# Performance work log

Hardware: AMD Instinct MI355X
Metric: run time of the kernel (lower is better)

The kernel has to match this reference:

```python
import jax, jax.numpy as jnp
import numpy as np

EMBED_DIM = 768
NUM_HEADS = 12
HEAD_DIM = EMBED_DIM // NUM_HEADS
WINDOW = 64
B, S = 2, 2048


def setup_inputs() -> dict:
    key = jax.random.key(0)
    ks = jax.random.split(key, 8)
    xavier = 0.1 * np.sqrt(6.0 / (EMBED_DIM + EMBED_DIM))  # xavier_uniform with gain=0.1
    def lin_w(k):
        return jax.random.uniform(k, (EMBED_DIM, EMBED_DIM), jnp.float32, -xavier, xavier)
    return {
        "query": jax.random.normal(ks[0], (B, S, EMBED_DIM), jnp.float32),
        "key": jax.random.normal(ks[1], (B, S, EMBED_DIM), jnp.float32),
        "value": jax.random.normal(ks[2], (B, S, EMBED_DIM), jnp.float32),
        "key_padding_mask": jnp.zeros((B, S), dtype=bool),
        "Wq": lin_w(ks[3]), "bq": jnp.zeros((EMBED_DIM,), jnp.float32),
        "Wk": lin_w(ks[4]), "bk": jnp.zeros((EMBED_DIM,), jnp.float32),
        "Wv": lin_w(ks[5]), "bv": jnp.zeros((EMBED_DIM,), jnp.float32),
        "Wo": lin_w(ks[6]), "bo": jnp.zeros((EMBED_DIM,), jnp.float32),
    }


def reference(query, key, value, key_padding_mask, Wq, bq, Wk, bk, Wv, bv, Wo, bo):
    Bsz, Sl, E = query.shape
    H, D = NUM_HEADS, HEAD_DIM

    def proj(x, W, b):  # nn.Linear: x @ W.T + b, then split heads -> [B,H,S,D]
        return (x @ W.T + b).reshape(Bsz, Sl, H, D).transpose(0, 2, 1, 3)

    q = proj(query, Wq, bq)
    k = proj(key, Wk, bk)
    v = proj(value, Wv, bv)

    scale = float(D) ** -0.5
    scores = jnp.einsum("bhqd,bhkd->bhqk", q, k) * scale  # [B,H,S,S]

    idx = jnp.arange(Sl)
    win_mask = jnp.abs(idx[:, None] - idx[None, :]) > WINDOW  # True = masked out
    scores = jnp.where(win_mask[None, None], -10000.0, scores)
    scores = jnp.where(key_padding_mask[:, None, None, :], -10000.0, scores)
    scores = jnp.where(jnp.isnan(scores), -10000.0, scores)

    attn = jax.nn.softmax(scores, axis=-1) + 1e-6
    attn = jnp.where(jnp.isnan(attn), 1.0 / Sl, attn)

    ctx = jnp.einsum("bhqk,bhkd->bhqd", attn, v)
    ctx = ctx.transpose(0, 2, 1, 3).reshape(Bsz, Sl, E)
    out = ctx @ Wo.T + bo
    out = jnp.where(jnp.isnan(out), value, out)
    return out, attn
```

## Files before the change

kernel.cpp:

```cpp
#include <hip/hip_runtime.h>
#include <hip/hip_bf16.h>

#define EMBED 768
#define NHEADS 12
#define HDIM 64
#define WIN 64
#define BATCH 2
#define SEQ 2048
#define MROWS (BATCH*SEQ)
#define NBH (BATCH*NHEADS)
#define QT 32
#define KP 160
#define KPAD 168
#define SPAD 164

typedef __attribute__((ext_vector_type(8))) short short8;
typedef __attribute__((ext_vector_type(4))) float f32x4;

__device__ __forceinline__ float bf2f(unsigned short u) {
    union { unsigned int i; float f; } z;
    z.i = ((unsigned int)u) << 16;
    return z.f;
}
__device__ __forceinline__ unsigned short f2bf(float f) {
    __hip_bfloat16 h = __float2bfloat16(f);
    return *reinterpret_cast<unsigned short*>(&h);
}

__device__ __forceinline__ void gload16(const void* g, void* l) {
    __builtin_amdgcn_global_load_lds(
        (const __attribute__((address_space(1))) unsigned int*)g,
        (__attribute__((address_space(3))) unsigned int*)l,
        16, 0, 0);
}

struct CvtArgs {
    const float* src[4];
    unsigned short* dst[4];
};

__global__ __launch_bounds__(256) void cvt_w(CvtArgs ca) {
    const int n4 = EMBED * EMBED / 4;
    const int bper = (n4 + 255) / 256;
    int seg = blockIdx.x / bper;
    int i = (blockIdx.x - seg * bper) * 256 + threadIdx.x;
    if (i < n4) {
        float4 v = reinterpret_cast<const float4*>(ca.src[seg])[i];
        ushort4 o;
        o.x = f2bf(v.x); o.y = f2bf(v.y); o.z = f2bf(v.z); o.w = f2bf(v.w);
        reinterpret_cast<ushort4*>(ca.dst[seg])[i] = o;
    }
}

struct GArgs {
    const void* A[3];
    const unsigned short* Bm[3];
    const float* bias[3];
    void* C[3];
};

template<int F32OUT, int F32A>
__global__ __launch_bounds__(256) void gemm_nt(GArgs ga, int M, int N, int K) {
    const int NPANEL = gridDim.y * gridDim.z;
    const int flat = (blockIdx.z * gridDim.y + blockIdx.y) * gridDim.x + blockIdx.x;
    const int xcd = flat & 7;
    const int j = flat >> 3;
    const int panel = xcd * (NPANEL >> 3) + j / gridDim.x;
    const int z = panel / gridDim.y;
    const int bm = (panel % gridDim.y) * 128;
    const int bn = (j % gridDim.x) * 128;

    const unsigned short* __restrict__ Bm = ga.Bm[z];
    const float* __restrict__ bias = ga.bias[z];

    __shared__ alignas(16) unsigned char AsRaw[F32A ? 128 * 32 * 4 : 128 * 32 * 2];
    __shared__ unsigned short Bs[128 * 32];

    const int tid = threadIdx.x;
    const int lane = tid & 63;
    const int wid = tid >> 6;
    const int wm = wid >> 1, wn = wid & 1;

    f32x4 acc[4][4] = {};

    const int fr = lane & 15;
    const int krow = (lane >> 4) * 8;

    for (int k0 = 0; k0 < K; k0 += 32) {
        if (F32A) {
            const float* Af = (const float*)ga.A[z];
            float* AsF = (float*)AsRaw;
#pragma unroll
            for (int it = 0; it < 4; ++it) {
                int idx = it * 256 + tid;
                int r = idx >> 3;
                int cc = idx & 7;
                int gcc = cc ^ (r & 7);
                gload16(Af + (size_t)(bm + r) * K + k0 + gcc * 4, &AsF[idx * 4]);
            }
        } else {
            const unsigned short* Ab = (const unsigned short*)ga.A[z];
#pragma unroll
            for (int it = 0; it < 2; ++it) {
                int idx = it * 256 + tid;
                int r = idx >> 2;
                int c = (idx & 3) * 8;
                gload16(Ab + (size_t)(bm + r) * K + k0 + c,
                        (unsigned short*)AsRaw + idx * 8);
            }
        }
#pragma unroll
        for (int it = 0; it < 2; ++it) {
            int idx = it * 256 + tid;
            int r = idx >> 2;
            int c = (idx & 3) * 8;
            gload16(Bm + (size_t)(bn + r) * K + k0 + c, &Bs[idx * 8]);
        }
        __syncthreads();

        short8 af[4], bfv[4];
#pragma unroll
        for (int mf = 0; mf < 4; ++mf) {
            int r = wm * 64 + mf * 16 + fr;
            if (F32A) {
                const float* AsF = (const float*)AsRaw;
                int kc0 = (lane >> 4) * 2;
                int s0 = kc0 ^ (r & 7);
                f32x4 v0 = *reinterpret_cast<const f32x4*>(&AsF[(r * 8 + s0) * 4]);
                f32x4 v1 = *reinterpret_cast<const f32x4*>(&AsF[(r * 8 + (s0 ^ 1)) * 4]);
                unsigned short* ou = reinterpret_cast<unsigned short*>(&af[mf]);
                ou[0] = f2bf(v0[0]); ou[1] = f2bf(v0[1]);
                ou[2] = f2bf(v0[2]); ou[3] = f2bf(v0[3]);
                ou[4] = f2bf(v1[0]); ou[5] = f2bf(v1[1]);
                ou[6] = f2bf(v1[2]); ou[7] = f2bf(v1[3]);
            } else {
                af[mf] = *reinterpret_cast<const short8*>(
                    (const unsigned short*)AsRaw + r * 32 + krow);
            }
        }
#pragma unroll
        for (int nf = 0; nf < 4; ++nf)
            bfv[nf] = *reinterpret_cast<const short8*>(&Bs[(wn * 64 + nf * 16 + fr) * 32 + krow]);
#pragma unroll
        for (int mf = 0; mf < 4; ++mf)
#pragma unroll
            for (int nf = 0; nf < 4; ++nf)
                acc[mf][nf] = __builtin_amdgcn_mfma_f32_16x16x32_bf16(
                    af[mf], bfv[nf], acc[mf][nf], 0, 0, 0);
        __syncthreads();
    }

    const int fq = lane >> 4;
#pragma unroll
    for (int mf = 0; mf < 4; ++mf)
#pragma unroll
        for (int nf = 0; nf < 4; ++nf) {
            int col = bn + wn * 64 + nf * 16 + fr;
            float bv = bias[col];
#pragma unroll
            for (int r = 0; r < 4; ++r) {
                int row = bm + wm * 64 + mf * 16 + fq * 4 + r;
                float v = acc[mf][nf][r] + bv;
                if (F32OUT)
                    reinterpret_cast<float*>(ga.C[z])[(size_t)row * N + col] = v;
                else
                    reinterpret_cast<unsigned short*>(ga.C[z])[(size_t)row * N + col] = f2bf(v);
            }
        }
}

__global__ __launch_bounds__(256) void sumv_kernel(const unsigned short* __restrict__ Vb,
                                                   float* __restrict__ sumV) {
    __shared__ float r[32][HDIM];
    const int bh = blockIdx.x;
    const int b = bh / NHEADS, h = bh % NHEADS;
    const int dg = (threadIdx.x & 7) * 8;
    const int r0 = threadIdx.x >> 3;
    float acc[8] = {};
    const unsigned short* vp = Vb + (size_t)(b * SEQ) * EMBED + h * HDIM + dg;
    for (int j = r0; j < SEQ; j += 32) {
        short8 v = *reinterpret_cast<const short8*>(vp + (size_t)j * EMBED);
#pragma unroll
        for (int e = 0; e < 8; ++e)
            acc[e] += bf2f(((const unsigned short*)&v)[e]);
    }
#pragma unroll
    for (int e = 0; e < 8; ++e) r[r0][dg + e] = acc[e];
    __syncthreads();
    if (threadIdx.x < HDIM) {
        float s = 0.f;
#pragma unroll
        for (int i = 0; i < 32; ++i) s += r[i][threadIdx.x];
        sumV[bh * HDIM + threadIdx.x] = s;
    }
}

__global__ __launch_bounds__(256, 3) void attn_mfma(
    const unsigned short* __restrict__ Q,
    const unsigned short* __restrict__ Kb,
    const unsigned short* __restrict__ Vb,
    const unsigned char* __restrict__ kpm,
    const float* __restrict__ sumV,
    float* __restrict__ attn_out,
    unsigned short* __restrict__ ctx) {
    const int flat = blockIdx.y * gridDim.x + blockIdx.x;
    const int g2 = (flat & 7) * 192 + (flat >> 3);
    const int bh = g2 >> 6;
    const int qt = g2 & 63;
    const int h = bh % NHEADS;
    const int b = bh / NHEADS;
    const int q0 = qt * QT;
    const int kstart = max(q0 - WIN, 0);

    __shared__ float Sf[QT][SPAD];
    __shared__ unsigned short Pb[QT][KPAD];
    __shared__ unsigned short Vt[HDIM][KPAD];

    const int tid = threadIdx.x;
    const int l = tid & 63;
    const int w = tid >> 6;
    const int fr = l & 15;
    const int ksl = (l >> 4) * 8;

    const size_t base = (size_t)(b * SEQ) * EMBED + h * HDIM;

    {
        const f32x4 fill = {1e-6f, 1e-6f, 1e-6f, 1e-6f};
#pragma unroll
        for (int rr = 0; rr < QT / 4; ++rr) {
            int row = w * (QT / 4) + rr;
            int qi = q0 + row;
            int blo = max(qi - WIN, 0);
            int bhi = min(qi + WIN, SEQ - 1);
            float* __restrict__ orow = attn_out + ((size_t)bh * SEQ + qi) * SEQ;
#pragma unroll
            for (int seg = 0; seg < SEQ / 256; ++seg) {
                if (seg * 256 + 255 >= blo && seg * 256 <= bhi) continue;
                __builtin_nontemporal_store(
                    fill, reinterpret_cast<f32x4*>(orow + seg * 256 + l * 4));
            }
        }
    }

    {
        const int mf = w >> 1;
        const int nt0 = (w & 1) * 5;

        const unsigned short* qrow = Q + base + (size_t)(q0 + mf * 16 + fr) * EMBED;
        short8 aq0 = *reinterpret_cast<const short8*>(qrow + ksl);
        short8 aq1 = *reinterpret_cast<const short8*>(qrow + 32 + ksl);

        f32x4 sacc[5] = {};
#pragma unroll
        for (int t = 0; t < 5; ++t) {
            int jg = kstart + (nt0 + t) * 16 + fr;
            int jc = min(jg, SEQ - 1);
            const unsigned short* krow = Kb + base + (size_t)jc * EMBED;
            short8 b0 = *reinterpret_cast<const short8*>(krow + ksl);
            short8 b1 = *reinterpret_cast<const short8*>(krow + 32 + ksl);
            sacc[t] = __builtin_amdgcn_mfma_f32_16x16x32_bf16(aq0, b0, sacc[t], 0, 0, 0);
            sacc[t] = __builtin_amdgcn_mfma_f32_16x16x32_bf16(aq1, b1, sacc[t], 0, 0, 0);
        }

#pragma unroll
        for (int t = 0; t < 5; ++t) {
            int col = (nt0 + t) * 16 + fr;
            int jg = kstart + col;
            bool jvalid = (jg < SEQ);
            bool mk = jvalid && kpm[b * SEQ + jg];
#pragma unroll
            for (int r = 0; r < 4; ++r) {
                int rowl = mf * 16 + (l >> 4) * 4 + r;
                int qi = q0 + rowl;
                float s = sacc[t][r] * 0.125f;
                if (mk) s = -10000.f;
                int dd = qi - jg;
                if (!jvalid || dd > WIN || dd < -WIN) s = -1e30f;
                Sf[rowl][col] = s;
            }
        }

#pragma unroll
        for (int pass = 0; pass < 5; ++pass) {
            int jrel = pass * 32 + (tid >> 3);
            int jg = kstart + jrel;
            int dg = (tid & 7) * 8;
            short8 v = {};
            if (jg < SEQ)
                v = *reinterpret_cast<const short8*>(Vb + base + (size_t)jg * EMBED + dg);
#pragma unroll
            for (int e = 0; e < 8; ++e)
                Vt[dg + e][jrel] = ((const unsigned short*)&v)[e];
        }
    }
    __syncthreads();

    {
        const int row = tid >> 3;
        const int cg = tid & 7;
        float e[KP / 8];
        float m = -1e30f;
#pragma unroll
        for (int i = 0; i < KP / 8; ++i) {
            float s = Sf[row][cg + i * 8];
            e[i] = s;
            m = fmaxf(m, s);
        }
#pragma unroll
        for (int off = 1; off < 8; off <<= 1) m = fmaxf(m, __shfl_xor(m, off));
        float sum = 0.f;
#pragma unroll
        for (int i = 0; i < KP / 8; ++i) {
            e[i] = __expf(e[i] - m);
            sum += e[i];
        }
#pragma unroll
        for (int off = 1; off < 8; off <<= 1) sum += __shfl_xor(sum, off);
        float inv = 1.f / sum;
#pragma unroll
        for (int i = 0; i < KP / 8; ++i) {
            float p = e[i] * inv;
            int col = cg + i * 8;
            Sf[row][col] = p;
            Pb[row][col] = f2bf(p);
        }
    }
    __syncthreads();

    {
#pragma unroll
        for (int rr = 0; rr < QT / 4; ++rr) {
            int row = w * (QT / 4) + rr;
            int qi = q0 + row;
            int blo = max(qi - WIN, 0);
            int bhi = min(qi + WIN, SEQ - 1);
            float* __restrict__ orow = attn_out + ((size_t)bh * SEQ + qi) * SEQ;
            int slo = blo >> 8;
            int shi = bhi >> 8;
            for (int seg = slo; seg <= shi; ++seg) {
                int c0 = seg * 256 + l * 4;
                f32x4 v = {1e-6f, 1e-6f, 1e-6f, 1e-6f};
#pragma unroll
                for (int e = 0; e < 4; ++e) {
                    int c = c0 + e;
                    if (c >= blo && c <= bhi) v[e] = Sf[row][c - kstart] + 1e-6f;
                }
                __builtin_nontemporal_store(v, reinterpret_cast<f32x4*>(orow + c0));
            }
        }
    }

    {
        const int mf = w >> 1;
        const int nfb = (w & 1) * 2;
        f32x4 oacc[2] = {};
#pragma unroll
        for (int kk = 0; kk < KP / 32; ++kk) {
            short8 a = *reinterpret_cast<const short8*>(&Pb[mf * 16 + fr][kk * 32 + ksl]);
#pragma unroll
            for (int n2 = 0; n2 < 2; ++n2) {
                short8 bv = *reinterpret_cast<const short8*>(&Vt[(nfb + n2) * 16 + fr][kk * 32 + ksl]);
                oacc[n2] = __builtin_amdgcn_mfma_f32_16x16x32_bf16(a, bv, oacc[n2], 0, 0, 0);
            }
        }
#pragma unroll
        for (int n2 = 0; n2 < 2; ++n2) {
            int d = (nfb + n2) * 16 + fr;
            float sv = 1e-6f * sumV[bh * HDIM + d];
#pragma unroll
            for (int r = 0; r < 4; ++r) {
                int rowl = mf * 16 + (l >> 4) * 4 + r;
                ctx[base + (size_t)(q0 + rowl) * EMBED + d] = f2bf(oacc[n2][r] + sv);
            }
        }
    }
}

extern "C" void kernel_launch(void* const* d_in, const int* in_sizes, int n_in,
                              void* d_out, int out_size, void* d_ws, size_t ws_size,
                              hipStream_t stream) {
    const float* q_in = (const float*)d_in[0];
    const float* k_in = (const float*)d_in[1];
    const float* v_in = (const float*)d_in[2];
    const unsigned char* kpm = (const unsigned char*)d_in[3];
    const float* Wq = (const float*)d_in[4];
    const float* bq = (const float*)d_in[5];
    const float* Wk = (const float*)d_in[6];
    const float* bk = (const float*)d_in[7];
    const float* Wv = (const float*)d_in[8];
    const float* bv = (const float*)d_in[9];
    const float* Wo = (const float*)d_in[10];
    const float* bo = (const float*)d_in[11];

    char* ws = (char*)d_ws;
    size_t off = 0;
    auto alloc = [&](size_t bytes) {
        void* p = ws + off;
        off += (bytes + 255) & ~255ULL;
        return p;
    };
    const size_t XB = (size_t)MROWS * EMBED * 2;
    const size_t WB = (size_t)EMBED * EMBED * 2;
    unsigned short* wqb = (unsigned short*)alloc(WB);
    unsigned short* wkb = (unsigned short*)alloc(WB);
    unsigned short* wvb = (unsigned short*)alloc(WB);
    unsigned short* wob = (unsigned short*)alloc(WB);
    unsigned short* Qb = (unsigned short*)alloc(XB);
    unsigned short* Kb = (unsigned short*)alloc(XB);
    unsigned short* Vb = (unsigned short*)alloc(XB);
    unsigned short* ctx = (unsigned short*)alloc(XB);
    float* sumV = (float*)alloc((size_t)NBH * HDIM * 4);

    float* out0 = (float*)d_out;
    float* attn_out = out0 + (size_t)MROWS * EMBED;

    {
        CvtArgs ca;
        ca.src[0] = Wq; ca.src[1] = Wk; ca.src[2] = Wv; ca.src[3] = Wo;
        ca.dst[0] = wqb; ca.dst[1] = wkb; ca.dst[2] = wvb; ca.dst[3] = wob;
        int bper = (EMBED * EMBED / 4 + 255) / 256;
        cvt_w<<<dim3(4 * bper), dim3(256), 0, stream>>>(ca);
    }

    {
        GArgs ga;
        ga.A[0] = q_in; ga.A[1] = k_in; ga.A[2] = v_in;
        ga.Bm[0] = wqb; ga.Bm[1] = wkb; ga.Bm[2] = wvb;
        ga.bias[0] = bq; ga.bias[1] = bk; ga.bias[2] = bv;
        ga.C[0] = Qb; ga.C[1] = Kb; ga.C[2] = Vb;
        gemm_nt<0, 1><<<dim3(EMBED / 128, MROWS / 128, 3), dim3(256), 0, stream>>>(
            ga, MROWS, EMBED, EMBED);
    }

    sumv_kernel<<<dim3(NBH), dim3(256), 0, stream>>>(Vb, sumV);

    attn_mfma<<<dim3(SEQ / QT, NBH), dim3(256), 0, stream>>>(
        Qb, Kb, Vb, kpm, sumV, attn_out, ctx);

    {
        GArgs ga;
        ga.A[0] = ctx;  ga.A[1] = ctx;  ga.A[2] = ctx;
        ga.Bm[0] = wob; ga.Bm[1] = wob; ga.Bm[2] = wob;
        ga.bias[0] = bo; ga.bias[1] = bo; ga.bias[2] = bo;
        ga.C[0] = out0; ga.C[1] = out0; ga.C[2] = out0;
        gemm_nt<1, 0><<<dim3(EMBED / 128, MROWS / 128, 1), dim3(256), 0, stream>>>(
            ga, MROWS, EMBED, EMBED);
    }
}
```

Baseline: 159.9 us.

## Move attention-matrix background fill into the QKV projection GEMM kernel

The constant 1e-6 fill of the full attention output is moved out of the attention kernel. The QKV GEMM blocks now grid-stride over the whole attn buffer with nontemporal stores after their epilogue, so this bandwidth-bound write can overlap with GEMM compute. The attention kernel then only writes the banded segments. In exchange the band region is written twice, and the GEMM kernel takes on a large memory-write tail. The sumV loads in the attention kernel are also hoisted to the start.

```diff
diff --git a/kernel.cpp b/kernel.cpp
--- a/kernel.cpp
+++ b/kernel.cpp
@@ -57,9 +57,10 @@
     const unsigned short* Bm[3];
     const float* bias[3];
     void* C[3];
+    float* fill_out;
 };
 
-template<int F32OUT, int F32A>
+template<int F32OUT, int F32A, int FILL>
 __global__ __launch_bounds__(256) void gemm_nt(GArgs ga, int M, int N, int K) {
     const int NPANEL = gridDim.y * gridDim.z;
     const int flat = (blockIdx.z * gridDim.y + blockIdx.y) * gridDim.x + blockIdx.x;
@@ -167,6 +168,15 @@
                     reinterpret_cast<unsigned short*>(ga.C[z])[(size_t)row * N + col] = f2bf(v);
             }
         }
+
+    if (FILL) {
+        const f32x4 fv = {1e-6f, 1e-6f, 1e-6f, 1e-6f};
+        const size_t FILLN = (size_t)NBH * SEQ * (SEQ / 4);
+        const size_t stride = 576 * 256;
+        f32x4* p = reinterpret_cast<f32x4*>(ga.fill_out);
+        for (size_t i = (size_t)flat * 256 + tid; i < FILLN; i += stride)
+            __builtin_nontemporal_store(fv, p + i);
+    }
 }
 
 __global__ __launch_bounds__(256) void sumv_kernel(const unsigned short* __restrict__ Vb,
@@ -224,23 +234,9 @@
 
     const size_t base = (size_t)(b * SEQ) * EMBED + h * HDIM;
 
-    {
-        const f32x4 fill = {1e-6f, 1e-6f, 1e-6f, 1e-6f};
-#pragma unroll
-        for (int rr = 0; rr < QT / 4; ++rr) {
-            int row = w * (QT / 4) + rr;
-            int qi = q0 + row;
-            int blo = max(qi - WIN, 0);
-            int bhi = min(qi + WIN, SEQ - 1);
-            float* __restrict__ orow = attn_out + ((size_t)bh * SEQ + qi) * SEQ;
-#pragma unroll
-            for (int seg = 0; seg < SEQ / 256; ++seg) {
-                if (seg * 256 + 255 >= blo && seg * 256 <= bhi) continue;
-                __builtin_nontemporal_store(
-                    fill, reinterpret_cast<f32x4*>(orow + seg * 256 + l * 4));
-            }
-        }
-    }
+    const int nfb_pre = (w & 1) * 2;
+    float sv0 = 1e-6f * sumV[bh * HDIM + nfb_pre * 16 + fr];
+    float sv1 = 1e-6f * sumV[bh * HDIM + (nfb_pre + 1) * 16 + fr];
 
     {
         const int mf = w >> 1;
@@ -352,21 +348,20 @@
 
     {
         const int mf = w >> 1;
-        const int nfb = (w & 1) * 2;
         f32x4 oacc[2] = {};
 #pragma unroll
         for (int kk = 0; kk < KP / 32; ++kk) {
             short8 a = *reinterpret_cast<const short8*>(&Pb[mf * 16 + fr][kk * 32 + ksl]);
 #pragma unroll
             for (int n2 = 0; n2 < 2; ++n2) {
-                short8 bv = *reinterpret_cast<const short8*>(&Vt[(nfb + n2) * 16 + fr][kk * 32 + ksl]);
+                short8 bv = *reinterpret_cast<const short8*>(&Vt[(nfb_pre + n2) * 16 + fr][kk * 32 + ksl]);
                 oacc[n2] = __builtin_amdgcn_mfma_f32_16x16x32_bf16(a, bv, oacc[n2], 0, 0, 0);
             }
         }
 #pragma unroll
         for (int n2 = 0; n2 < 2; ++n2) {
-            int d = (nfb + n2) * 16 + fr;
-            float sv = 1e-6f * sumV[bh * HDIM + d];
+            int d = (nfb_pre + n2) * 16 + fr;
+            float sv = (n2 == 0) ? sv0 : sv1;
 #pragma unroll
             for (int r = 0; r < 4; ++r) {
                 int rowl = mf * 16 + (l >> 4) * 4 + r;
@@ -428,7 +423,8 @@
         ga.Bm[0] = wqb; ga.Bm[1] = wkb; ga.Bm[2] = wvb;
         ga.bias[0] = bq; ga.bias[1] = bk; ga.bias[2] = bv;
         ga.C[0] = Qb; ga.C[1] = Kb; ga.C[2] = Vb;
-        gemm_nt<0, 1><<<dim3(EMBED / 128, MROWS / 128, 3), dim3(256), 0, stream>>>(
+        ga.fill_out = attn_out;
+        gemm_nt<0, 1, 1><<<dim3(EMBED / 128, MROWS / 128, 3), dim3(256), 0, stream>>>(
             ga, MROWS, EMBED, EMBED);
     }
 
@@ -443,7 +439,8 @@
         ga.Bm[0] = wob; ga.Bm[1] = wob; ga.Bm[2] = wob;
         ga.bias[0] = bo; ga.bias[1] = bo; ga.bias[2] = bo;
         ga.C[0] = out0; ga.C[1] = out0; ga.C[2] = out0;
-        gemm_nt<1, 0><<<dim3(EMBED / 128, MROWS / 128, 1), dim3(256), 0, stream>>>(
+        ga.fill_out = nullptr;
+        gemm_nt<1, 0, 0><<<dim3(EMBED / 128, MROWS / 128, 1), dim3(256), 0, stream>>>(
             ga, MROWS, EMBED, EMBED);
     }
 }
```

New measurement: 188.9 us. 1.18x slower.
